# Kernel optimization log

Measured on AMD Instinct MI355X. Metric: run time of the kernel, lower is better.

Reference implementation:

```python
import jax, jax.numpy as jnp
import numpy as np

B, N = 65536, 128  # batch of point clouds, points per cloud

def setup_inputs() -> dict:
    key = jax.random.key(0)
    k1, k2 = jax.random.split(key)
    x = jax.random.normal(k1, (B, N, 3), dtype=jnp.float32)
    y = jax.random.normal(k2, (B, N, 3), dtype=jnp.float32)
    return {"x": x, "y": y}

def reference(x, y):
    # zero-center both point clouds
    xc = x - x.mean(axis=-2, keepdims=True)
    yc = y - y.mean(axis=-2, keepdims=True)
    # batched 3x3 covariance: C[..., j, k] = sum_i xc[..., i, j] * yc[..., i, k]
    C = jnp.einsum('...ij,...ik->...jk', xc, yc)
    # torch.linalg.svd returns (U, S, Vh); original code names Vh as V and forms R = U @ Vh
    U, _, Vh = jnp.linalg.svd(C)
    R = jnp.einsum('...ij,...jk->...ik', U, Vh)
    x_aligned = jnp.einsum('...ij,...jk->...ik', xc, R)
    # mean square deviation over all batch, point, and coordinate dims
    return jnp.mean((x_aligned - yc) ** 2)
```

## Files before the change

### kernel.cpp

```cpp
#include <hip/hip_runtime.h>
#include <math.h>


#define NPTS 128
#define WPB 4
#define BLOCKS 2048
#define TOTAL_WAVES (BLOCKS * WPB)
#define TILE_F4 192
#define BUF_F4 (2 * TILE_F4)

__device__ __forceinline__ void stage_tile(const float4* __restrict__ x4,
                                           const float4* __restrict__ y4,
                                           size_t tile, float4* buf, int lane) {
    const size_t base = tile * TILE_F4;
    #pragma unroll
    for (int r = 0; r < 3; ++r) {
        __builtin_amdgcn_global_load_lds(
            (const __attribute__((address_space(1))) void*)(x4 + base + r * 64 + lane),
            (__attribute__((address_space(3))) void*)(buf + r * 64), 16, 0, 0);
        __builtin_amdgcn_global_load_lds(
            (const __attribute__((address_space(1))) void*)(y4 + base + r * 64 + lane),
            (__attribute__((address_space(3))) void*)(buf + TILE_F4 + r * 64), 16, 0, 0);
    }
}

template<int CTRL, int RMASK>
__device__ __forceinline__ float dpp_add(float v) {
    int t = __builtin_amdgcn_update_dpp(0, __builtin_bit_cast(int, v),
                                        CTRL, RMASK, 0xF, true);
    return v + __builtin_bit_cast(float, t);
}

__device__ __forceinline__ float acos_fast(float x) {
    float ax = fabsf(x);
    float p = fmaf(ax, -0.0187293f, 0.0742610f);
    p = fmaf(ax, p, -0.2121144f);
    p = fmaf(ax, p, 1.5707288f);
    float s = __builtin_amdgcn_sqrtf(fmaxf(1.0f - ax, 0.0f));
    float r = s * p;
    return (x < 0.0f) ? (3.14159265358979f - r) : r;
}

__global__ __launch_bounds__(256, 3) void kabsch_kernel(
        const float4* __restrict__ x4, const float4* __restrict__ y4,
        float* __restrict__ out, float scale, int tilesPerWave) {
    __shared__ float4 smem[WPB][2][BUF_F4];
    __shared__ float wsum[WPB];

    const int tid  = threadIdx.x;
    const int lane = tid & 63;
    const int wave = tid >> 6;
    const int w    = blockIdx.x * WPB + wave;

    float4* buf0 = &smem[wave][0][0];
    float4* buf1 = &smem[wave][1][0];

    stage_tile(x4, y4, (size_t)w, buf0, lane);

    const int g   = lane >> 5;
    const int sub = lane & 31;
    const float invN = 1.0f / (float)NPTS;

    float wave_acc = 0.f;

    for (int t = 0; t < tilesPerWave; ++t) {
        float4* cur = (t & 1) ? buf1 : buf0;
        float4* nxt = (t & 1) ? buf0 : buf1;

        asm volatile("s_waitcnt vmcnt(0)" ::: "memory");

        const float4* xs = cur + g * 96 + sub * 3;
        const float4* ys = cur + TILE_F4 + g * 96 + sub * 3;
        float4 xv0 = xs[0], xv1 = xs[1], xv2 = xs[2];
        float4 yv0 = ys[0], yv1 = ys[1], yv2 = ys[2];

        if (t + 1 < tilesPerWave)
            stage_tile(x4, y4, (size_t)w + (size_t)(t + 1) * TOTAL_WAVES, nxt, lane);

        float fx[12], fy[12];
        fx[0]=xv0.x; fx[1]=xv0.y; fx[2]=xv0.z; fx[3]=xv0.w;
        fx[4]=xv1.x; fx[5]=xv1.y; fx[6]=xv1.z; fx[7]=xv1.w;
        fx[8]=xv2.x; fx[9]=xv2.y; fx[10]=xv2.z; fx[11]=xv2.w;
        fy[0]=yv0.x; fy[1]=yv0.y; fy[2]=yv0.z; fy[3]=yv0.w;
        fy[4]=yv1.x; fy[5]=yv1.y; fy[6]=yv1.z; fy[7]=yv1.w;
        fy[8]=yv2.x; fy[9]=yv2.y; fy[10]=yv2.z; fy[11]=yv2.w;

        float sx0=0.f,sx1=0.f,sx2=0.f, sy0=0.f,sy1=0.f,sy2=0.f, qq=0.f;
        float c00=0.f,c01=0.f,c02=0.f,c10=0.f,c11=0.f,c12=0.f,
              c20=0.f,c21=0.f,c22=0.f;

        #pragma unroll
        for (int p = 0; p < 4; ++p) {
            float px0=fx[3*p], px1=fx[3*p+1], px2=fx[3*p+2];
            float py0=fy[3*p], py1=fy[3*p+1], py2=fy[3*p+2];
            sx0+=px0; sx1+=px1; sx2+=px2;
            sy0+=py0; sy1+=py1; sy2+=py2;
            qq = fmaf(px0,px0,fmaf(px1,px1,fmaf(px2,px2,qq)));
            qq = fmaf(py0,py0,fmaf(py1,py1,fmaf(py2,py2,qq)));
            c00=fmaf(px0,py0,c00); c01=fmaf(px0,py1,c01); c02=fmaf(px0,py2,c02);
            c10=fmaf(px1,py0,c10); c11=fmaf(px1,py1,c11); c12=fmaf(px1,py2,c12);
            c20=fmaf(px2,py0,c20); c21=fmaf(px2,py1,c21); c22=fmaf(px2,py2,c22);
        }

#define STAGE(C, M) \
        sx0=dpp_add<C,M>(sx0); sx1=dpp_add<C,M>(sx1); sx2=dpp_add<C,M>(sx2); \
        sy0=dpp_add<C,M>(sy0); sy1=dpp_add<C,M>(sy1); sy2=dpp_add<C,M>(sy2); \
        qq =dpp_add<C,M>(qq);                                                \
        c00=dpp_add<C,M>(c00); c01=dpp_add<C,M>(c01); c02=dpp_add<C,M>(c02); \
        c10=dpp_add<C,M>(c10); c11=dpp_add<C,M>(c11); c12=dpp_add<C,M>(c12); \
        c20=dpp_add<C,M>(c20); c21=dpp_add<C,M>(c21); c22=dpp_add<C,M>(c22);
        STAGE(0xB1, 0xF)
        STAGE(0x4E, 0xF)
        STAGE(0x141, 0xF)
        STAGE(0x140, 0xF)
        STAGE(0x142, 0xA)
#undef STAGE

        float C00 = c00 - sx0*sy0*invN, C01 = c01 - sx0*sy1*invN, C02 = c02 - sx0*sy2*invN;
        float C10 = c10 - sx1*sy0*invN, C11 = c11 - sx1*sy1*invN, C12 = c12 - sx1*sy2*invN;
        float C20 = c20 - sx2*sy0*invN, C21 = c21 - sx2*sy1*invN, C22 = c22 - sx2*sy2*invN;
        float Sxy = qq - (sx0*sx0 + sx1*sx1 + sx2*sx2
                        + sy0*sy0 + sy1*sy1 + sy2*sy2) * invN;

        float a00 = C00*C00 + C10*C10 + C20*C20;
        float a01 = C00*C01 + C10*C11 + C20*C21;
        float a02 = C00*C02 + C10*C12 + C20*C22;
        float a11 = C01*C01 + C11*C11 + C21*C21;
        float a12 = C01*C02 + C11*C12 + C21*C22;
        float a22 = C02*C02 + C12*C12 + C22*C22;

        float q = (a00 + a11 + a22) * (1.0f / 3.0f);
        float b00 = a00 - q, b11 = a11 - q, b22 = a22 - q;
        float p2 = (b00*b00 + b11*b11 + b22*b22
                    + 2.0f * (a01*a01 + a02*a02 + a12*a12)) * (1.0f / 6.0f);
        float p = __builtin_amdgcn_sqrtf(fmaxf(p2, 0.0f));
        float detB = b00 * (b11*b22 - a12*a12)
                   - a01 * (a01*b22 - a12*a02)
                   + a02 * (a01*a12 - b11*a02);
        float r = 0.5f * detB * __builtin_amdgcn_rcpf(p * p * p);
        r = fminf(1.0f, fmaxf(-1.0f, r));
        float phi_rev = acos_fast(r) * 0.05305164769729845f;
        float two_p = 2.0f * p;
        float l1 = q + two_p * __builtin_amdgcn_cosf(phi_rev);
        float l3 = q + two_p * __builtin_amdgcn_cosf(phi_rev + 0.33333333333f);
        float l2 = 3.0f * q - l1 - l3;
        float nuc = __builtin_amdgcn_sqrtf(fmaxf(l1, 0.0f))
                  + __builtin_amdgcn_sqrtf(fmaxf(l2, 0.0f))
                  + __builtin_amdgcn_sqrtf(fmaxf(l3, 0.0f));

        wave_acc += Sxy - 2.0f * nuc;
    }

    float t0 = __builtin_bit_cast(float, __builtin_amdgcn_readlane(
                   __builtin_bit_cast(int, wave_acc), 31));
    float t1 = __builtin_bit_cast(float, __builtin_amdgcn_readlane(
                   __builtin_bit_cast(int, wave_acc), 63));
    if (lane == 0) wsum[wave] = t0 + t1;
    __syncthreads();
    if (tid == 0) {
        float tsum = (wsum[0] + wsum[1] + wsum[2] + wsum[3]) * scale;
        atomicAdd(out, tsum);
    }
}

extern "C" void kernel_launch(void* const* d_in, const int* in_sizes, int n_in,
                              void* d_out, int out_size, void* d_ws, size_t ws_size,
                              hipStream_t stream) {
    const float4* x4 = (const float4*)d_in[0];
    const float4* y4 = (const float4*)d_in[1];
    float* out = (float*)d_out;

    const int B = in_sizes[0] / (NPTS * 3);
    const int totalTiles = B / 2;
    const int tilesPerWave = totalTiles / TOTAL_WAVES;
    const float scale = 1.0f / ((float)B * (float)NPTS * 3.0f);

    hipMemsetAsync(out, 0, sizeof(float), stream);
    kabsch_kernel<<<BLOCKS, WPB * 64, 0, stream>>>(x4, y4, out, scale, tilesPerWave);
}
```

Before: 216.7 us.

## Replace LDS async staging with register-prefetched direct global loads

Drops the global_load_lds double-buffered shared-memory staging and instead loads each lane's three float4s of x and y straight into registers, prefetching the next tile while the current one is computed. This removes the LDS round trip and the full vmcnt(0) wait each iteration. The grid is halved to 1024 blocks, so each wave handles twice as many tiles, and the launch-bounds occupancy hint rises from 3 to 4 blocks per CU. The trade-off is more live registers from the prefetch and fewer waves in flight to hide memory latency.

```diff
diff --git a/kernel.cpp b/kernel.cpp
--- a/kernel.cpp
+++ b/kernel.cpp
@@ -4,25 +4,9 @@
 
 #define NPTS 128
 #define WPB 4
-#define BLOCKS 2048
+#define BLOCKS 1024
 #define TOTAL_WAVES (BLOCKS * WPB)
 #define TILE_F4 192
-#define BUF_F4 (2 * TILE_F4)
-
-__device__ __forceinline__ void stage_tile(const float4* __restrict__ x4,
-                                           const float4* __restrict__ y4,
-                                           size_t tile, float4* buf, int lane) {
-    const size_t base = tile * TILE_F4;
-    #pragma unroll
-    for (int r = 0; r < 3; ++r) {
-        __builtin_amdgcn_global_load_lds(
-            (const __attribute__((address_space(1))) void*)(x4 + base + r * 64 + lane),
-            (__attribute__((address_space(3))) void*)(buf + r * 64), 16, 0, 0);
-        __builtin_amdgcn_global_load_lds(
-            (const __attribute__((address_space(1))) void*)(y4 + base + r * 64 + lane),
-            (__attribute__((address_space(3))) void*)(buf + TILE_F4 + r * 64), 16, 0, 0);
-    }
-}
 
 template<int CTRL, int RMASK>
 __device__ __forceinline__ float dpp_add(float v) {
@@ -41,66 +25,48 @@
     return (x < 0.0f) ? (3.14159265358979f - r) : r;
 }
 
-__global__ __launch_bounds__(256, 3) void kabsch_kernel(
+__global__ __launch_bounds__(256, 4) void kabsch_kernel(
         const float4* __restrict__ x4, const float4* __restrict__ y4,
         float* __restrict__ out, float scale, int tilesPerWave) {
-    __shared__ float4 smem[WPB][2][BUF_F4];
     __shared__ float wsum[WPB];
 
     const int tid  = threadIdx.x;
     const int lane = tid & 63;
     const int wave = tid >> 6;
     const int w    = blockIdx.x * WPB + wave;
+    const float invN = 1.0f / (float)NPTS;
 
-    float4* buf0 = &smem[wave][0][0];
-    float4* buf1 = &smem[wave][1][0];
+    const size_t base0 = (size_t)w * TILE_F4 + lane * 3;
 
-    stage_tile(x4, y4, (size_t)w, buf0, lane);
-
-    const int g   = lane >> 5;
-    const int sub = lane & 31;
-    const float invN = 1.0f / (float)NPTS;
+    float4 ax0 = x4[base0], ax1 = x4[base0 + 1], ax2 = x4[base0 + 2];
+    float4 ay0 = y4[base0], ay1 = y4[base0 + 1], ay2 = y4[base0 + 2];
 
     float wave_acc = 0.f;
 
+    #pragma unroll 2
     for (int t = 0; t < tilesPerWave; ++t) {
-        float4* cur = (t & 1) ? buf1 : buf0;
-        float4* nxt = (t & 1) ? buf0 : buf1;
-
-        asm volatile("s_waitcnt vmcnt(0)" ::: "memory");
-
-        const float4* xs = cur + g * 96 + sub * 3;
-        const float4* ys = cur + TILE_F4 + g * 96 + sub * 3;
-        float4 xv0 = xs[0], xv1 = xs[1], xv2 = xs[2];
-        float4 yv0 = ys[0], yv1 = ys[1], yv2 = ys[2];
-
-        if (t + 1 < tilesPerWave)
-            stage_tile(x4, y4, (size_t)w + (size_t)(t + 1) * TOTAL_WAVES, nxt, lane);
-
-        float fx[12], fy[12];
-        fx[0]=xv0.x; fx[1]=xv0.y; fx[2]=xv0.z; fx[3]=xv0.w;
-        fx[4]=xv1.x; fx[5]=xv1.y; fx[6]=xv1.z; fx[7]=xv1.w;
-        fx[8]=xv2.x; fx[9]=xv2.y; fx[10]=xv2.z; fx[11]=xv2.w;
-        fy[0]=yv0.x; fy[1]=yv0.y; fy[2]=yv0.z; fy[3]=yv0.w;
-        fy[4]=yv1.x; fy[5]=yv1.y; fy[6]=yv1.z; fy[7]=yv1.w;
-        fy[8]=yv2.x; fy[9]=yv2.y; fy[10]=yv2.z; fy[11]=yv2.w;
+        const size_t nb = (t + 1 < tilesPerWave)
+            ? base0 + (size_t)(t + 1) * TOTAL_WAVES * TILE_F4 : base0;
+        float4 bx0 = x4[nb], bx1 = x4[nb + 1], bx2 = x4[nb + 2];
+        float4 by0 = y4[nb], by1 = y4[nb + 1], by2 = y4[nb + 2];
 
         float sx0=0.f,sx1=0.f,sx2=0.f, sy0=0.f,sy1=0.f,sy2=0.f, qq=0.f;
         float c00=0.f,c01=0.f,c02=0.f,c10=0.f,c11=0.f,c12=0.f,
               c20=0.f,c21=0.f,c22=0.f;
-
-        #pragma unroll
-        for (int p = 0; p < 4; ++p) {
-            float px0=fx[3*p], px1=fx[3*p+1], px2=fx[3*p+2];
-            float py0=fy[3*p], py1=fy[3*p+1], py2=fy[3*p+2];
-            sx0+=px0; sx1+=px1; sx2+=px2;
-            sy0+=py0; sy1+=py1; sy2+=py2;
-            qq = fmaf(px0,px0,fmaf(px1,px1,fmaf(px2,px2,qq)));
-            qq = fmaf(py0,py0,fmaf(py1,py1,fmaf(py2,py2,qq)));
-            c00=fmaf(px0,py0,c00); c01=fmaf(px0,py1,c01); c02=fmaf(px0,py2,c02);
-            c10=fmaf(px1,py0,c10); c11=fmaf(px1,py1,c11); c12=fmaf(px1,py2,c12);
-            c20=fmaf(px2,py0,c20); c21=fmaf(px2,py1,c21); c22=fmaf(px2,py2,c22);
-        }
+#define ACC(px0,px1,px2,py0,py1,py2) do {                                  \
+        sx0+=px0; sx1+=px1; sx2+=px2;                                      \
+        sy0+=py0; sy1+=py1; sy2+=py2;                                      \
+        qq = fmaf(px0,px0,fmaf(px1,px1,fmaf(px2,px2,qq)));                 \
+        qq = fmaf(py0,py0,fmaf(py1,py1,fmaf(py2,py2,qq)));                 \
+        c00=fmaf(px0,py0,c00); c01=fmaf(px0,py1,c01); c02=fmaf(px0,py2,c02); \
+        c10=fmaf(px1,py0,c10); c11=fmaf(px1,py1,c11); c12=fmaf(px1,py2,c12); \
+        c20=fmaf(px2,py0,c20); c21=fmaf(px2,py1,c21); c22=fmaf(px2,py2,c22); \
+    } while (0)
+        ACC(ax0.x, ax0.y, ax0.z,  ay0.x, ay0.y, ay0.z);
+        ACC(ax0.w, ax1.x, ax1.y,  ay0.w, ay1.x, ay1.y);
+        ACC(ax1.z, ax1.w, ax2.x,  ay1.z, ay1.w, ay2.x);
+        ACC(ax2.y, ax2.z, ax2.w,  ay2.y, ay2.z, ay2.w);
+#undef ACC
 
 #define STAGE(C, M) \
         sx0=dpp_add<C,M>(sx0); sx1=dpp_add<C,M>(sx1); sx2=dpp_add<C,M>(sx2); \
@@ -149,6 +115,9 @@
                   + __builtin_amdgcn_sqrtf(fmaxf(l3, 0.0f));
 
         wave_acc += Sxy - 2.0f * nuc;
+
+        ax0 = bx0; ax1 = bx1; ax2 = bx2;
+        ay0 = by0; ay1 = by1; ay2 = by2;
     }
 
     float t0 = __builtin_bit_cast(float, __builtin_amdgcn_readlane(
```

Result: no change. 214.3 us (-1.1%).
